# Optimization experiments

Hardware: AMD Instinct MI355X
Metric: run time of the kernel (lower is better)

The kernel has to match this reference:

```python
import jax, jax.numpy as jnp
import numpy as np
import math

N_HEAD = 16
N_EMBD = 1024


def setup_inputs() -> dict:
    key = jax.random.key(0)
    ks = jax.random.split(key, 8)
    B, T, C = 2, 2048, N_EMBD
    x = jax.random.normal(ks[0], (B, T, C), dtype=jnp.float32)
    # Linear weights stored as [in, out] (transposed vs torch's [out, in])
    W_attn = jax.random.normal(ks[1], (C, 3 * C), dtype=jnp.float32) * (1.0 / math.sqrt(C))
    b_attn = jnp.zeros((3 * C,), dtype=jnp.float32)
    W_proj = jax.random.normal(ks[2], (C, C), dtype=jnp.float32) * (1.0 / math.sqrt(C))
    b_proj = jnp.zeros((C,), dtype=jnp.float32)
    threshold = jnp.full((N_HEAD,), 0.01, dtype=jnp.float32)
    leak = jnp.full((N_HEAD,), 2.0, dtype=jnp.float32)
    steepness = jnp.full((N_HEAD,), 2.0, dtype=jnp.float32)
    return {"x": x, "W_attn": W_attn, "b_attn": b_attn, "W_proj": W_proj,
            "b_proj": b_proj, "threshold": threshold, "leak": leak,
            "steepness": steepness}


def reference(x, W_attn, b_attn, W_proj, b_proj, threshold, leak, steepness):
    B, T, C = x.shape
    H = N_HEAD
    hd = C // H
    qkv = x @ W_attn + b_attn  # [B, T, 3C]
    q, k, v = jnp.split(qkv, 3, axis=-1)
    # [B, H, T, hd]
    q = q.reshape(B, T, H, hd).transpose(0, 2, 1, 3)
    k = k.reshape(B, T, H, hd).transpose(0, 2, 1, 3)
    v = v.reshape(B, T, H, hd).transpose(0, 2, 1, 3)

    att = jnp.einsum('bhqd,bhkd->bhqk', q, k) * (1.0 / math.sqrt(hd))
    causal = jnp.tril(jnp.ones((T, T), dtype=bool))  # [T, T]
    att = jnp.where(causal[None, None, :, :], att, -jnp.inf)

    probs = jax.nn.softmax(att, axis=-1)  # [B, H, T, T]
    thr = (jnp.abs(threshold) * 0.1).reshape(1, H, 1, 1)
    lk = jax.nn.sigmoid(leak).reshape(1, H, 1, 1)
    st = jax.nn.softplus(steepness).reshape(1, H, 1, 1)
    fire = jax.nn.sigmoid(st * (probs - thr))
    lif_w = fire + lk * (1.0 - fire)
    mod = probs * lif_w
    mod = mod / (jnp.sum(mod, axis=-1, keepdims=True) + 1e-8)

    y = jnp.einsum('bhqk,bhkd->bhqd', mod, v)  # [B, H, T, hd]
    y = y.transpose(0, 2, 1, 3).reshape(B, T, C)
    return y @ W_proj + b_proj
```

## Files before the change

### kernel.cpp

```cpp
#include <hip/hip_runtime.h>
#include <hip/hip_bf16.h>
#include <math.h>

#define NHEAD 16
#define HD 64
#define TSEQ 2048
#define CEMB 1024

typedef __attribute__((ext_vector_type(8))) short short8;
typedef __attribute__((ext_vector_type(4))) float f32x4;
typedef __attribute__((ext_vector_type(16))) float f32x16;

__device__ inline unsigned short f2bf(float f) {
  union { float f; unsigned u; } x; x.f = f;
  unsigned r = x.u + 0x7FFFu + ((x.u >> 16) & 1u);
  return (unsigned short)(r >> 16);
}

__device__ inline unsigned pk2(float a, float b) {
  __hip_bfloat162 t = __float22bfloat162_rn(make_float2(a, b));
  union { __hip_bfloat162 v; unsigned u; } c; c.v = t;
  return c.u;
}

__device__ inline float ex2(float x) {
#if __has_builtin(__builtin_amdgcn_exp2f)
  return __builtin_amdgcn_exp2f(x);
#else
  float r; asm("v_exp_f32 %0, %1" : "=v"(r) : "v"(x)); return r;
#endif
}

__device__ inline void gload16(const void* g, void* l) {
  __builtin_amdgcn_global_load_lds(
      (const __attribute__((address_space(1))) unsigned int*)g,
      (__attribute__((address_space(3))) unsigned int*)l, 16, 0, 0);
}

__global__ __launch_bounds__(256) void castx(const float* __restrict__ in,
                                             unsigned short* __restrict__ out) {
  int i = blockIdx.x * 256 + threadIdx.x;
  float4 v = ((const float4*)in)[i];
  ushort4 o;
  o.x = f2bf(v.x); o.y = f2bf(v.y); o.z = f2bf(v.z); o.w = f2bf(v.w);
  ((ushort4*)out)[i] = o;
}

__global__ __launch_bounds__(256) void transW(const float* __restrict__ W,
                                              unsigned short* __restrict__ Wt,
                                              int N) {
  __shared__ float t[64][65];
  const int tid = threadIdx.x;
  const int rb = blockIdx.y * 64;
  const int cb = blockIdx.x * 64;
#pragma unroll
  for (int i = 0; i < 16; ++i) {
    int idx = i * 256 + tid, r = idx >> 6, cl = idx & 63;
    t[r][cl] = W[(size_t)(rb + r) * N + cb + cl];
  }
  __syncthreads();
#pragma unroll
  for (int i = 0; i < 16; ++i) {
    int idx = i * 256 + tid, r = idx >> 6, cl = idx & 63;
    Wt[(size_t)(cb + r) * 1024 + rb + cl] = f2bf(t[cl][r]);
  }
}

template <int MODE>
__global__ __launch_bounds__(256) void mm128(const unsigned short* __restrict__ A,
                                             const unsigned short* __restrict__ Bt,
                                             const float* __restrict__ bias,
                                             void* __restrict__ out0,
                                             unsigned short* __restrict__ ko,
                                             unsigned short* __restrict__ vto) {
  __shared__ __align__(16) unsigned char Asm[16384];
  __shared__ __align__(16) unsigned char Bsm[16384];
  const int tid = threadIdx.x;
  const int lane = tid & 63;
  const int w = tid >> 6;
  const int wm = w >> 1, wn = w & 1;
  const int c = lane & 15, g = lane >> 4;
  const int rowbase = blockIdx.y * 128;
  const int colbase = blockIdx.x * 128;

  f32x4 acc[4][4];
#pragma unroll
  for (int m = 0; m < 4; ++m)
#pragma unroll
    for (int n = 0; n < 4; ++n) acc[m][n] = (f32x4){0.f, 0.f, 0.f, 0.f};

  const unsigned char* Ab = (const unsigned char*)(A + (size_t)rowbase * 1024);
  const unsigned char* Bb = (const unsigned char*)(Bt + (size_t)colbase * 1024);
  const int swz = (c & 7) << 4;

  for (int kt = 0; kt < 16; ++kt) {
    __syncthreads();
#pragma unroll
    for (int it = 0; it < 4; ++it) {
      const int L = it * 4096 + tid * 16;
      const int row = L >> 7;
      const int sc = (L & 127) ^ ((row & 7) << 4);
      gload16(Ab + (size_t)row * 2048 + kt * 128 + sc, Asm + L);
      gload16(Bb + (size_t)row * 2048 + kt * 128 + sc, Bsm + L);
    }
    __syncthreads();
#pragma unroll
    for (int ks = 0; ks < 2; ++ks) {
      const int cb = ks * 64 + 16 * g;
      short8 af[4], bf[4];
#pragma unroll
      for (int m = 0; m < 4; ++m)
        af[m] = *(const short8*)(Asm + (wm * 64 + m * 16 + c) * 128 + (cb ^ swz));
#pragma unroll
      for (int n = 0; n < 4; ++n)
        bf[n] = *(const short8*)(Bsm + (wn * 64 + n * 16 + c) * 128 + (cb ^ swz));
#pragma unroll
      for (int m = 0; m < 4; ++m)
#pragma unroll
        for (int n = 0; n < 4; ++n)
          acc[m][n] = __builtin_amdgcn_mfma_f32_16x16x32_bf16(af[m], bf[n], acc[m][n], 0, 0, 0);
    }
  }

#pragma unroll
  for (int m = 0; m < 4; ++m) {
    const int rw = rowbase + wm * 64 + m * 16 + 4 * g;
#pragma unroll
    for (int n = 0; n < 4; ++n) {
      const int col = colbase + wn * 64 + n * 16 + c;
      const float bz = bias[col];
      if (MODE == 0) {
        unsigned short* qo = (unsigned short*)out0;
        const int sel = col >> 10, cc = col & 1023, hh = cc >> 6, d = cc & 63;
#pragma unroll
        for (int r = 0; r < 4; ++r) {
          const int row = rw + r;
          const int b = row >> 11, t = row & 2047;
          const float val = acc[m][n][r] + bz;
          const size_t bh = (size_t)(b * NHEAD + hh);
          if (sel == 0)
            qo[(bh * TSEQ + t) * HD + d] = f2bf(val * 0.18033688011112042f);
          else if (sel == 1)
            ko[(bh * TSEQ + t) * HD + d] = f2bf(val);
          else
            vto[(bh * HD + d) * TSEQ + t] = f2bf(val);
        }
      } else {
        float* out = (float*)out0;
#pragma unroll
        for (int r = 0; r < 4; ++r)
          out[(size_t)(rw + r) * 1024 + col] = acc[m][n][r] + bz;
      }
    }
  }
}

__global__ __launch_bounds__(256) void lif_sw(
    const unsigned short* __restrict__ qb,
    const unsigned short* __restrict__ kb,
    const unsigned short* __restrict__ vtb,
    const float* __restrict__ thr_p, const float* __restrict__ leak_p,
    const float* __restrict__ steep_p,
    unsigned short* __restrict__ y) {
  __shared__ float obuf[4][32][33];
  __shared__ float lbuf[4][32];
  __shared__ float msbuf[4][32];

  const int bh = blockIdx.x;
  const int qt = 63 - blockIdx.y;
  const int h = bh & (NHEAD - 1);
  const int b = bh >> 4;
  const int tid = threadIdx.x;
  const int s = tid >> 6;
  const int lane = tid & 63;
  const int qv = lane & 31;
  const int hi = lane >> 5;
  const int klb = 4 * hi;
  const int qbase = qt * 32;

  const int nt = qt + 1;
  const int nt4 = (nt + 3) >> 2;
  const int t0 = s * nt4;
  const int t1 = min(t0 + nt4, nt);

  const unsigned short* qp = qb + (size_t)bh * TSEQ * HD;
  const unsigned short* kp = kb + (size_t)bh * TSEQ * HD;
  const unsigned short* vp = vtb + (size_t)bh * HD * TSEQ;

  const float thr = fabsf(thr_p[h]) * 0.1f;
  const float lk = 1.f / (1.f + __expf(-leak_p[h]));
  const float st = log1pf(__expf(steep_p[h]));
  const float stc = st * 1.44269504088896f;
  const float stthr2 = stc * thr;
  const float omlk = 1.f - lk;

  short8 qf[4];
#pragma unroll
  for (int kk = 0; kk < 4; ++kk)
    qf[kk] = *(const short8*)(qp + (size_t)(qbase + qv) * HD + 16 * kk + 8 * hi);

  float l_ = 0.f;
  for (int t = t0; t < t1; ++t) {
    const unsigned short* kt = kp + (size_t)t * 32 * HD;
    f32x16 sv = {};
#pragma unroll
    for (int kk = 0; kk < 4; ++kk) {
      short8 ka = *(const short8*)(kt + (size_t)qv * HD + 16 * kk + 8 * hi);
      sv = __builtin_amdgcn_mfma_f32_32x32x16_bf16(ka, qf[kk], sv, 0, 0, 0);
    }
    if (t == qt) {
#pragma unroll
      for (int j = 0; j < 16; ++j)
        if ((j & 3) + 8 * (j >> 2) + klb > qv) sv[j] = -1e30f;
    }
#pragma unroll
    for (int j = 0; j < 16; ++j) l_ += ex2(sv[j]);
  }
  l_ += __shfl_xor(l_, 32, 64);
  if (hi == 0) lbuf[s][qv] = l_;
  __syncthreads();
  const float l = (lbuf[0][qv] + lbuf[1][qv]) + (lbuf[2][qv] + lbuf[3][qv]);
  const float stli2 = stc / l;

  f32x16 o0 = {}, o1 = {};
  float ms = 0.f;
  for (int t = t0; t < t1; ++t) {
    const unsigned short* kt = kp + (size_t)t * 32 * HD;
    f32x16 sv = {};
#pragma unroll
    for (int kk = 0; kk < 4; ++kk) {
      short8 ka = *(const short8*)(kt + (size_t)qv * HD + 16 * kk + 8 * hi);
      sv = __builtin_amdgcn_mfma_f32_32x32x16_bf16(ka, qf[kk], sv, 0, 0, 0);
    }
    short8 va00 = *(const short8*)(vp + (size_t)(qv) * TSEQ + t * 32 + 8 * hi);
    short8 va01 = *(const short8*)(vp + (size_t)(qv) * TSEQ + t * 32 + 16 + 8 * hi);
    short8 va10 = *(const short8*)(vp + (size_t)(32 + qv) * TSEQ + t * 32 + 8 * hi);
    short8 va11 = *(const short8*)(vp + (size_t)(32 + qv) * TSEQ + t * 32 + 16 + 8 * hi);

    if (t == qt) {
#pragma unroll
      for (int j = 0; j < 16; ++j)
        if ((j & 3) + 8 * (j >> 2) + klb > qv) sv[j] = -1e30f;
    }
    unsigned cw[8];
#pragma unroll
    for (int jj = 0; jj < 8; ++jj) {
      float e0 = ex2(sv[2 * jj]);
      float e1 = ex2(sv[2 * jj + 1]);
      float u0 = ex2(fmaf(-stli2, e0, stthr2));
      float u1 = ex2(fmaf(-stli2, e1, stthr2));
      float f0 = __builtin_amdgcn_rcpf(1.f + u0);
      float f1 = __builtin_amdgcn_rcpf(1.f + u1);
      float m0 = e0 * fmaf(omlk, f0, lk);
      float m1 = e1 * fmaf(omlk, f1, lk);
      ms += m0;
      ms += m1;
      cw[jj] = pk2(m0, m1);
    }
    asm("v_permlane32_swap_b32 %0, %1" : "+v"(cw[0]), "+v"(cw[2]));
    asm("v_permlane32_swap_b32 %0, %1" : "+v"(cw[1]), "+v"(cw[3]));
    asm("v_permlane32_swap_b32 %0, %1" : "+v"(cw[4]), "+v"(cw[6]));
    asm("v_permlane32_swap_b32 %0, %1" : "+v"(cw[5]), "+v"(cw[7]));
    union { unsigned u[4]; short8 v; } B0, B1;
    B0.u[0] = cw[0]; B0.u[1] = cw[1]; B0.u[2] = cw[2]; B0.u[3] = cw[3];
    B1.u[0] = cw[4]; B1.u[1] = cw[5]; B1.u[2] = cw[6]; B1.u[3] = cw[7];

    o0 = __builtin_amdgcn_mfma_f32_32x32x16_bf16(va00, B0.v, o0, 0, 0, 0);
    o0 = __builtin_amdgcn_mfma_f32_32x32x16_bf16(va01, B1.v, o0, 0, 0, 0);
    o1 = __builtin_amdgcn_mfma_f32_32x32x16_bf16(va10, B0.v, o1, 0, 0, 0);
    o1 = __builtin_amdgcn_mfma_f32_32x32x16_bf16(va11, B1.v, o1, 0, 0, 0);
  }

  ms += __shfl_xor(ms, 32, 64);
  if (hi == 0) msbuf[s][qv] = ms;

#pragma unroll
  for (int j = 0; j < 16; ++j) {
    const int dl = (j & 3) + 8 * (j >> 2) + klb;
    obuf[s][qv][dl] = o0[j];
  }
  __syncthreads();
  {
    const int dl = tid & 31;
    const int qq = tid >> 5;
#pragma unroll
    for (int it = 0; it < 4; ++it) {
      const int q = qq * 4 + it;
      const float acc = (obuf[0][q][dl] + obuf[1][q][dl]) +
                        (obuf[2][q][dl] + obuf[3][q][dl]);
      const float mt = (msbuf[0][q] + msbuf[1][q]) + (msbuf[2][q] + msbuf[3][q]);
      y[((size_t)(b * TSEQ) + qbase + q) * CEMB + h * HD + dl] =
          f2bf(acc / (mt + 1e-8f));
    }
  }
  __syncthreads();
#pragma unroll
  for (int j = 0; j < 16; ++j) {
    const int dl = (j & 3) + 8 * (j >> 2) + klb;
    obuf[s][qv][dl] = o1[j];
  }
  __syncthreads();
  {
    const int dl = tid & 31;
    const int qq = tid >> 5;
#pragma unroll
    for (int it = 0; it < 4; ++it) {
      const int q = qq * 4 + it;
      const float acc = (obuf[0][q][dl] + obuf[1][q][dl]) +
                        (obuf[2][q][dl] + obuf[3][q][dl]);
      const float mt = (msbuf[0][q] + msbuf[1][q]) + (msbuf[2][q] + msbuf[3][q]);
      y[((size_t)(b * TSEQ) + qbase + q) * CEMB + h * HD + 32 + dl] =
          f2bf(acc / (mt + 1e-8f));
    }
  }
}

extern "C" void kernel_launch(void* const* d_in, const int* in_sizes, int n_in,
                              void* d_out, int out_size, void* d_ws, size_t ws_size,
                              hipStream_t stream) {
  const float* x      = (const float*)d_in[0];
  const float* W_attn = (const float*)d_in[1];
  const float* b_attn = (const float*)d_in[2];
  const float* W_proj = (const float*)d_in[3];
  const float* b_proj = (const float*)d_in[4];
  const float* thr    = (const float*)d_in[5];
  const float* leak   = (const float*)d_in[6];
  const float* steep  = (const float*)d_in[7];
  float* out = (float*)d_out;

  unsigned short* xb   = (unsigned short*)d_ws;
  unsigned short* Wat  = xb + (size_t)4096 * 1024;
  unsigned short* Wpt  = Wat + (size_t)3072 * 1024;
  unsigned short* qws  = Wpt + (size_t)1024 * 1024;
  unsigned short* kws  = qws + (size_t)32 * 2048 * 64;
  unsigned short* vtws = kws + (size_t)32 * 2048 * 64;
  unsigned short* yb   = vtws + (size_t)32 * 2048 * 64;

  castx<<<4096, 256, 0, stream>>>(x, xb);
  transW<<<dim3(48, 16), 256, 0, stream>>>(W_attn, Wat, 3072);
  transW<<<dim3(16, 16), 256, 0, stream>>>(W_proj, Wpt, 1024);
  mm128<0><<<dim3(24, 32), 256, 0, stream>>>(xb, Wat, b_attn, qws, kws, vtws);
  lif_sw<<<dim3(32, 64), 256, 0, stream>>>(qws, kws, vtws, thr, leak, steep, yb);
  mm128<1><<<dim3(8, 32), 256, 0, stream>>>(yb, Wpt, b_proj, out, nullptr, nullptr);
}
```

Baseline: 192.9 us.

## Pair causal query tiles per block to balance attention work

Each attention block now processes two query tiles, 63-y and y, so every block does the same total number of causal key tiles. The grid shrinks from 2048 to 1024 blocks. This targets the load imbalance and tail effect of triangular causal work. The cost is fewer blocks for latency hiding, plus an extra barrier per half. Pointer arithmetic is also hoisted into per-lane base pointers.

```diff
diff --git a/kernel.cpp b/kernel.cpp
--- a/kernel.cpp
+++ b/kernel.cpp
@@ -167,7 +167,6 @@
   __shared__ float msbuf[4][32];
 
   const int bh = blockIdx.x;
-  const int qt = 63 - blockIdx.y;
   const int h = bh & (NHEAD - 1);
   const int b = bh >> 4;
   const int tid = threadIdx.x;
@@ -176,12 +175,6 @@
   const int qv = lane & 31;
   const int hi = lane >> 5;
   const int klb = 4 * hi;
-  const int qbase = qt * 32;
-
-  const int nt = qt + 1;
-  const int nt4 = (nt + 3) >> 2;
-  const int t0 = s * nt4;
-  const int t1 = min(t0 + nt4, nt);
 
   const unsigned short* qp = qb + (size_t)bh * TSEQ * HD;
   const unsigned short* kp = kb + (size_t)bh * TSEQ * HD;
@@ -194,123 +187,139 @@
   const float stthr2 = stc * thr;
   const float omlk = 1.f - lk;
 
-  short8 qf[4];
-#pragma unroll
-  for (int kk = 0; kk < 4; ++kk)
-    qf[kk] = *(const short8*)(qp + (size_t)(qbase + qv) * HD + 16 * kk + 8 * hi);
-
-  float l_ = 0.f;
-  for (int t = t0; t < t1; ++t) {
-    const unsigned short* kt = kp + (size_t)t * 32 * HD;
-    f32x16 sv = {};
-#pragma unroll
-    for (int kk = 0; kk < 4; ++kk) {
-      short8 ka = *(const short8*)(kt + (size_t)qv * HD + 16 * kk + 8 * hi);
-      sv = __builtin_amdgcn_mfma_f32_32x32x16_bf16(ka, qf[kk], sv, 0, 0, 0);
-    }
-    if (t == qt) {
-#pragma unroll
-      for (int j = 0; j < 16; ++j)
-        if ((j & 3) + 8 * (j >> 2) + klb > qv) sv[j] = -1e30f;
-    }
-#pragma unroll
-    for (int j = 0; j < 16; ++j) l_ += ex2(sv[j]);
-  }
-  l_ += __shfl_xor(l_, 32, 64);
-  if (hi == 0) lbuf[s][qv] = l_;
-  __syncthreads();
-  const float l = (lbuf[0][qv] + lbuf[1][qv]) + (lbuf[2][qv] + lbuf[3][qv]);
-  const float stli2 = stc / l;
-
-  f32x16 o0 = {}, o1 = {};
-  float ms = 0.f;
-  for (int t = t0; t < t1; ++t) {
-    const unsigned short* kt = kp + (size_t)t * 32 * HD;
-    f32x16 sv = {};
-#pragma unroll
-    for (int kk = 0; kk < 4; ++kk) {
-      short8 ka = *(const short8*)(kt + (size_t)qv * HD + 16 * kk + 8 * hi);
-      sv = __builtin_amdgcn_mfma_f32_32x32x16_bf16(ka, qf[kk], sv, 0, 0, 0);
-    }
-    short8 va00 = *(const short8*)(vp + (size_t)(qv) * TSEQ + t * 32 + 8 * hi);
-    short8 va01 = *(const short8*)(vp + (size_t)(qv) * TSEQ + t * 32 + 16 + 8 * hi);
-    short8 va10 = *(const short8*)(vp + (size_t)(32 + qv) * TSEQ + t * 32 + 8 * hi);
-    short8 va11 = *(const short8*)(vp + (size_t)(32 + qv) * TSEQ + t * 32 + 16 + 8 * hi);
-
-    if (t == qt) {
-#pragma unroll
-      for (int j = 0; j < 16; ++j)
-        if ((j & 3) + 8 * (j >> 2) + klb > qv) sv[j] = -1e30f;
-    }
-    unsigned cw[8];
-#pragma unroll
-    for (int jj = 0; jj < 8; ++jj) {
-      float e0 = ex2(sv[2 * jj]);
-      float e1 = ex2(sv[2 * jj + 1]);
-      float u0 = ex2(fmaf(-stli2, e0, stthr2));
-      float u1 = ex2(fmaf(-stli2, e1, stthr2));
-      float f0 = __builtin_amdgcn_rcpf(1.f + u0);
-      float f1 = __builtin_amdgcn_rcpf(1.f + u1);
-      float m0 = e0 * fmaf(omlk, f0, lk);
-      float m1 = e1 * fmaf(omlk, f1, lk);
-      ms += m0;
-      ms += m1;
-      cw[jj] = pk2(m0, m1);
-    }
-    asm("v_permlane32_swap_b32 %0, %1" : "+v"(cw[0]), "+v"(cw[2]));
-    asm("v_permlane32_swap_b32 %0, %1" : "+v"(cw[1]), "+v"(cw[3]));
-    asm("v_permlane32_swap_b32 %0, %1" : "+v"(cw[4]), "+v"(cw[6]));
-    asm("v_permlane32_swap_b32 %0, %1" : "+v"(cw[5]), "+v"(cw[7]));
-    union { unsigned u[4]; short8 v; } B0, B1;
-    B0.u[0] = cw[0]; B0.u[1] = cw[1]; B0.u[2] = cw[2]; B0.u[3] = cw[3];
-    B1.u[0] = cw[4]; B1.u[1] = cw[5]; B1.u[2] = cw[6]; B1.u[3] = cw[7];
-
-    o0 = __builtin_amdgcn_mfma_f32_32x32x16_bf16(va00, B0.v, o0, 0, 0, 0);
-    o0 = __builtin_amdgcn_mfma_f32_32x32x16_bf16(va01, B1.v, o0, 0, 0, 0);
-    o1 = __builtin_amdgcn_mfma_f32_32x32x16_bf16(va10, B0.v, o1, 0, 0, 0);
-    o1 = __builtin_amdgcn_mfma_f32_32x32x16_bf16(va11, B1.v, o1, 0, 0, 0);
-  }
-
-  ms += __shfl_xor(ms, 32, 64);
-  if (hi == 0) msbuf[s][qv] = ms;
-
-#pragma unroll
-  for (int j = 0; j < 16; ++j) {
-    const int dl = (j & 3) + 8 * (j >> 2) + klb;
-    obuf[s][qv][dl] = o0[j];
-  }
-  __syncthreads();
-  {
-    const int dl = tid & 31;
-    const int qq = tid >> 5;
-#pragma unroll
-    for (int it = 0; it < 4; ++it) {
-      const int q = qq * 4 + it;
-      const float acc = (obuf[0][q][dl] + obuf[1][q][dl]) +
-                        (obuf[2][q][dl] + obuf[3][q][dl]);
-      const float mt = (msbuf[0][q] + msbuf[1][q]) + (msbuf[2][q] + msbuf[3][q]);
-      y[((size_t)(b * TSEQ) + qbase + q) * CEMB + h * HD + dl] =
-          f2bf(acc / (mt + 1e-8f));
-    }
-  }
-  __syncthreads();
-#pragma unroll
-  for (int j = 0; j < 16; ++j) {
-    const int dl = (j & 3) + 8 * (j >> 2) + klb;
-    obuf[s][qv][dl] = o1[j];
-  }
-  __syncthreads();
-  {
-    const int dl = tid & 31;
-    const int qq = tid >> 5;
-#pragma unroll
-    for (int it = 0; it < 4; ++it) {
-      const int q = qq * 4 + it;
-      const float acc = (obuf[0][q][dl] + obuf[1][q][dl]) +
-                        (obuf[2][q][dl] + obuf[3][q][dl]);
-      const float mt = (msbuf[0][q] + msbuf[1][q]) + (msbuf[2][q] + msbuf[3][q]);
-      y[((size_t)(b * TSEQ) + qbase + q) * CEMB + h * HD + 32 + dl] =
-          f2bf(acc / (mt + 1e-8f));
+  const unsigned short* kpl  = kp + (size_t)qv * HD + 8 * hi;
+  const unsigned short* vpl0 = vp + (size_t)qv * TSEQ + 8 * hi;
+  const unsigned short* vpl1 = vp + (size_t)(32 + qv) * TSEQ + 8 * hi;
+
+  for (int half = 0; half < 2; ++half) {
+    const int qt = half == 0 ? 63 - blockIdx.y : blockIdx.y;
+    const int qbase = qt * 32;
+    const int nt = qt + 1;
+    const int nt4 = (nt + 3) >> 2;
+    const int t0 = s * nt4;
+    const int t1 = min(t0 + nt4, nt);
+
+    __syncthreads();
+
+    const unsigned short* qpl = qp + (size_t)(qbase + qv) * HD + 8 * hi;
+    const short8 qf0 = *(const short8*)(qpl);
+    const short8 qf1 = *(const short8*)(qpl + 16);
+    const short8 qf2 = *(const short8*)(qpl + 32);
+    const short8 qf3 = *(const short8*)(qpl + 48);
+
+    float l_ = 0.f;
+    for (int t = t0; t < t1; ++t) {
+      const unsigned short* kt = kpl + (size_t)t * (32 * HD);
+      f32x16 sv = {};
+      sv = __builtin_amdgcn_mfma_f32_32x32x16_bf16(*(const short8*)(kt), qf0, sv, 0, 0, 0);
+      sv = __builtin_amdgcn_mfma_f32_32x32x16_bf16(*(const short8*)(kt + 16), qf1, sv, 0, 0, 0);
+      sv = __builtin_amdgcn_mfma_f32_32x32x16_bf16(*(const short8*)(kt + 32), qf2, sv, 0, 0, 0);
+      sv = __builtin_amdgcn_mfma_f32_32x32x16_bf16(*(const short8*)(kt + 48), qf3, sv, 0, 0, 0);
+      if (t == qt) {
+#pragma unroll
+        for (int j = 0; j < 16; ++j)
+          if ((j & 3) + 8 * (j >> 2) + klb > qv) sv[j] = -1e30f;
+      }
+#pragma unroll
+      for (int j = 0; j < 16; ++j) l_ += ex2(sv[j]);
+    }
+    l_ += __shfl_xor(l_, 32, 64);
+    if (hi == 0) lbuf[s][qv] = l_;
+    __syncthreads();
+    const float l = (lbuf[0][qv] + lbuf[1][qv]) + (lbuf[2][qv] + lbuf[3][qv]);
+    const float stli2 = stc / l;
+
+    f32x16 o0 = {}, o1 = {};
+    float ms = 0.f;
+    for (int t = t0; t < t1; ++t) {
+      const unsigned short* kt = kpl + (size_t)t * (32 * HD);
+      f32x16 sv = {};
+      sv = __builtin_amdgcn_mfma_f32_32x32x16_bf16(*(const short8*)(kt), qf0, sv, 0, 0, 0);
+      sv = __builtin_amdgcn_mfma_f32_32x32x16_bf16(*(const short8*)(kt + 16), qf1, sv, 0, 0, 0);
+      sv = __builtin_amdgcn_mfma_f32_32x32x16_bf16(*(const short8*)(kt + 32), qf2, sv, 0, 0, 0);
+      sv = __builtin_amdgcn_mfma_f32_32x32x16_bf16(*(const short8*)(kt + 48), qf3, sv, 0, 0, 0);
+      const unsigned short* v0 = vpl0 + t * 32;
+      const unsigned short* v1 = vpl1 + t * 32;
+      short8 va00 = *(const short8*)(v0);
+      short8 va01 = *(const short8*)(v0 + 16);
+      short8 va10 = *(const short8*)(v1);
+      short8 va11 = *(const short8*)(v1 + 16);
+
+      if (t == qt) {
+#pragma unroll
+        for (int j = 0; j < 16; ++j)
+          if ((j & 3) + 8 * (j >> 2) + klb > qv) sv[j] = -1e30f;
+      }
+      unsigned cw[8];
+#pragma unroll
+      for (int jj = 0; jj < 8; ++jj) {
+        float e0 = ex2(sv[2 * jj]);
+        float e1 = ex2(sv[2 * jj + 1]);
+        float u0 = ex2(fmaf(-stli2, e0, stthr2));
+        float u1 = ex2(fmaf(-stli2, e1, stthr2));
+        float f0 = __builtin_amdgcn_rcpf(1.f + u0);
+        float f1 = __builtin_amdgcn_rcpf(1.f + u1);
+        float m0 = e0 * fmaf(omlk, f0, lk);
+        float m1 = e1 * fmaf(omlk, f1, lk);
+        ms += m0;
+        ms += m1;
+        cw[jj] = pk2(m0, m1);
+      }
+      asm("v_permlane32_swap_b32 %0, %1" : "+v"(cw[0]), "+v"(cw[2]));
+      asm("v_permlane32_swap_b32 %0, %1" : "+v"(cw[1]), "+v"(cw[3]));
+      asm("v_permlane32_swap_b32 %0, %1" : "+v"(cw[4]), "+v"(cw[6]));
+      asm("v_permlane32_swap_b32 %0, %1" : "+v"(cw[5]), "+v"(cw[7]));
+      union { unsigned u[4]; short8 v; } B0, B1;
+      B0.u[0] = cw[0]; B0.u[1] = cw[1]; B0.u[2] = cw[2]; B0.u[3] = cw[3];
+      B1.u[0] = cw[4]; B1.u[1] = cw[5]; B1.u[2] = cw[6]; B1.u[3] = cw[7];
+
+      o0 = __builtin_amdgcn_mfma_f32_32x32x16_bf16(va00, B0.v, o0, 0, 0, 0);
+      o0 = __builtin_amdgcn_mfma_f32_32x32x16_bf16(va01, B1.v, o0, 0, 0, 0);
+      o1 = __builtin_amdgcn_mfma_f32_32x32x16_bf16(va10, B0.v, o1, 0, 0, 0);
+      o1 = __builtin_amdgcn_mfma_f32_32x32x16_bf16(va11, B1.v, o1, 0, 0, 0);
+    }
+
+    ms += __shfl_xor(ms, 32, 64);
+    if (hi == 0) msbuf[s][qv] = ms;
+
+#pragma unroll
+    for (int j = 0; j < 16; ++j) {
+      const int dl = (j & 3) + 8 * (j >> 2) + klb;
+      obuf[s][qv][dl] = o0[j];
+    }
+    __syncthreads();
+    {
+      const int dl = tid & 31;
+      const int qq = tid >> 5;
+#pragma unroll
+      for (int it = 0; it < 4; ++it) {
+        const int q = qq * 4 + it;
+        const float acc = (obuf[0][q][dl] + obuf[1][q][dl]) +
+                          (obuf[2][q][dl] + obuf[3][q][dl]);
+        const float mt = (msbuf[0][q] + msbuf[1][q]) + (msbuf[2][q] + msbuf[3][q]);
+        y[((size_t)(b * TSEQ) + qbase + q) * CEMB + h * HD + dl] =
+            f2bf(acc / (mt + 1e-8f));
+      }
+    }
+    __syncthreads();
+#pragma unroll
+    for (int j = 0; j < 16; ++j) {
+      const int dl = (j & 3) + 8 * (j >> 2) + klb;
+      obuf[s][qv][dl] = o1[j];
+    }
+    __syncthreads();
+    {
+      const int dl = tid & 31;
+      const int qq = tid >> 5;
+#pragma unroll
+      for (int it = 0; it < 4; ++it) {
+        const int q = qq * 4 + it;
+        const float acc = (obuf[0][q][dl] + obuf[1][q][dl]) +
+                          (obuf[2][q][dl] + obuf[3][q][dl]);
+        const float mt = (msbuf[0][q] + msbuf[1][q]) + (msbuf[2][q] + msbuf[3][q]);
+        y[((size_t)(b * TSEQ) + qbase + q) * CEMB + h * HD + 32 + dl] =
+            f2bf(acc / (mt + 1e-8f));
+      }
     }
   }
 }
@@ -340,6 +349,6 @@
   transW<<<dim3(48, 16), 256, 0, stream>>>(W_attn, Wat, 3072);
   transW<<<dim3(16, 16), 256, 0, stream>>>(W_proj, Wpt, 1024);
   mm128<0><<<dim3(24, 32), 256, 0, stream>>>(xb, Wat, b_attn, qws, kws, vtws);
-  lif_sw<<<dim3(32, 64), 256, 0, stream>>>(qws, kws, vtws, thr, leak, steep, yb);
+  lif_sw<<<dim3(32, 32), 256, 0, stream>>>(qws, kws, vtws, thr, leak, steep, yb);
   mm128<1><<<dim3(8, 32), 256, 0, stream>>>(yb, Wpt, b_proj, out, nullptr, nullptr);
 }
```

After: 193.2 us. No clear change (+0.1%).
